# Optimization experiments

Hardware: AMD Instinct MI355X
Metric: run time of the kernel (lower is better)

Reference implementation:

```python
import jax, jax.numpy as jnp
import numpy as np

B, T, D, U = 32, 2048, 512, 512


def setup_inputs() -> dict:
    key = jax.random.key(0)
    ks = jax.random.split(key, 6)
    scale = 0.05
    return {
        "values": jax.random.normal(ks[0], (B, T, D), dtype=jnp.float32),
        "query": jax.random.normal(ks[1], (B, D), dtype=jnp.float32),
        "W1_w": jax.random.normal(ks[2], (D, U), dtype=jnp.float32) * scale,
        "W1_b": jnp.zeros((U,), dtype=jnp.float32),
        "W2_w": jax.random.normal(ks[3], (D, U), dtype=jnp.float32) * scale,
        "W2_b": jnp.zeros((U,), dtype=jnp.float32),
        "V_w": jax.random.normal(ks[4], (U, 1), dtype=jnp.float32) * scale,
        "V_b": jnp.zeros((1,), dtype=jnp.float32),
    }


def reference(values, query, W1_w, W1_b, W2_w, W2_b, V_w, V_b):
    # values: [B, T, D]; query: [B, D]
    proj_v = jnp.einsum("btd,du->btu", values, W1_w) + W1_b          # [B, T, U]
    proj_q = (query @ W2_w + W2_b)[:, None, :]                        # [B, 1, U]
    score = jnp.tanh(proj_v + proj_q) @ V_w + V_b                     # [B, T, 1]
    attention_weights = jax.nn.softmax(score, axis=1)                 # [B, T, 1]
    context_vector = jnp.sum(attention_weights * values, axis=1)      # [B, D]
    return context_vector, attention_weights
```

## Files before the change

kernel.cpp:

```cpp
#include <hip/hip_runtime.h>
#include <hip/hip_bf16.h>
#include <stdint.h>


#define B_DIM 32
#define T_DIM 2048
#define D_DIM 512
#define U_DIM 512
#define M_DIM (B_DIM * T_DIM)

typedef short bf16x8 __attribute__((ext_vector_type(8)));
typedef float f32x4 __attribute__((ext_vector_type(4)));

__device__ __forceinline__ float fast_tanh(float x) {
    float e = __expf(2.0f * x);
    return 1.0f - __fdividef(2.0f, e + 1.0f);
}

__device__ __forceinline__ short bf16r(float x) {
    unsigned u = __float_as_uint(x);
    u += 0x7fffu + ((u >> 16) & 1u);
    return (short)(u >> 16);
}

__device__ __forceinline__ bf16x8 pack8(float4 a, float4 b) {
    union { __hip_bfloat162 h[4]; bf16x8 v; } u;
    u.h[0] = __float22bfloat162_rn(make_float2(a.x, a.y));
    u.h[1] = __float22bfloat162_rn(make_float2(a.z, a.w));
    u.h[2] = __float22bfloat162_rn(make_float2(b.x, b.y));
    u.h[3] = __float22bfloat162_rn(make_float2(b.z, b.w));
    return u.v;
}

__device__ __forceinline__ void g2lds16(const void* g, void* lds) {
    auto gp = reinterpret_cast<const __attribute__((address_space(1))) unsigned int*>(
        reinterpret_cast<uintptr_t>(g));
    auto lp = reinterpret_cast<__attribute__((address_space(3))) unsigned int*>(
        (unsigned int)(uintptr_t)lds);
    __builtin_amdgcn_global_load_lds(gp, lp, 16, 0, 0);
}


__global__ void prep_kernel(const float* __restrict__ W1_w,
                            const float* __restrict__ W1_b,
                            const float* __restrict__ W2_w,
                            const float* __restrict__ W2_b,
                            const float* __restrict__ query,
                            unsigned short* __restrict__ W1T,
                            float* __restrict__ qb) {
    __shared__ float red[256];
    const int tid = threadIdx.x;
    if (blockIdx.x < 128) {
        int n = blockIdx.x * 256 + tid;
        int uu    = n & 255;
        int kc    = (n >> 8) & 3;
        int kstep = (n >> 10) & 15;
        int ut    = n >> 14;
        int u  = ut * 256 + uu;
        int k0 = kstep * 32 + kc * 8;
        bf16x8 pk;
#pragma unroll
        for (int j = 0; j < 8; ++j)
            pk[j] = bf16r(W1_w[(size_t)(k0 + j) * U_DIM + u]);
        ((bf16x8*)W1T)[n] = pk;
    } else {
        int bid = blockIdx.x - 128;
        int b  = bid >> 3;
        int ug = bid & 7;
        int u  = ug * 64 + (tid & 63);
        int dq = tid >> 6;
        const float* q  = query + b * D_DIM + dq * 128;
        const float* w2 = W2_w + (size_t)(dq * 128) * U_DIM + u;
        float acc = 0.f;
#pragma unroll 8
        for (int d = 0; d < 128; ++d)
            acc += q[d] * w2[(size_t)d * U_DIM];
        red[tid] = acc;
        __syncthreads();
        if (tid < 64) {
            qb[b * U_DIM + u] = red[tid] + red[tid + 64] + red[tid + 128]
                              + red[tid + 192] + W2_b[u] + W1_b[u];
        }
    }
}

__global__ __launch_bounds__(256, 2) void score_kernel(
        const float* __restrict__ values,
        const unsigned short* __restrict__ W1T,
        const float* __restrict__ qb,
        const float* __restrict__ Vw,
        float* __restrict__ sP) {
    __shared__ __align__(16) unsigned char smem[16384];

    const int tid  = threadIdx.x;
    const int lane = tid & 63;
    const int w    = tid >> 6;
    const int l15  = lane & 15;
    const int quad = lane >> 4;
    const int wr   = w >> 1, wc = w & 1;
    const int ut    = blockIdx.x & 1;
    const int mtile = blockIdx.x >> 1;
    const int mb    = mtile * 64;
    const int b     = mb >> 11;

    const float* arow0 = values + (size_t)(mb + wr * 32 + l15) * D_DIM + quad * 8;
    const float* arow1 = arow0 + 16 * D_DIM;

    f32x4 acc[2][8] = {};

    for (int ks = 0; ks < 16; ++ks) {
        float4 a00 = *(const float4*)(arow0 + ks * 32);
        float4 a01 = *(const float4*)(arow0 + ks * 32 + 4);
        float4 a10 = *(const float4*)(arow1 + ks * 32);
        float4 a11 = *(const float4*)(arow1 + ks * 32 + 4);

        __syncthreads();
        const unsigned short* src = W1T + (size_t)(ut * 16 + ks) * 8192;
#pragma unroll
        for (int i = 0; i < 4; ++i) {
            int unit = i * 256 + w * 64 + lane;
            g2lds16(src + (size_t)unit * 8, smem + unit * 16);
        }
        __syncthreads();

        bf16x8 a0 = pack8(a00, a01);
        bf16x8 a1 = pack8(a10, a11);
        const unsigned char* bbase = smem + (size_t)(quad * 256 + wc * 128 + l15) * 16;
#pragma unroll
        for (int ui = 0; ui < 8; ++ui) {
            bf16x8 bf = *(const bf16x8*)(bbase + ui * 256);
            acc[0][ui] = __builtin_amdgcn_mfma_f32_16x16x32_bf16(a0, bf, acc[0][ui], 0, 0, 0);
            acc[1][ui] = __builtin_amdgcn_mfma_f32_16x16x32_bf16(a1, bf, acc[1][ui], 0, 0, 0);
        }
    }

    const int ub = ut * 256 + wc * 128 + l15;
    float sm[2][4] = {};
#pragma unroll
    for (int ui = 0; ui < 8; ++ui) {
        const int u = ub + ui * 16;
        const float qv = qb[b * U_DIM + u];
        const float vw = Vw[u];
#pragma unroll
        for (int mt = 0; mt < 2; ++mt)
#pragma unroll
            for (int r = 0; r < 4; ++r)
                sm[mt][r] += fast_tanh(acc[mt][ui][r] + qv) * vw;
    }
#pragma unroll
    for (int mt = 0; mt < 2; ++mt)
#pragma unroll
        for (int r = 0; r < 4; ++r) {
            float v = sm[mt][r];
            v += __shfl_xor(v, 1, 64);
            v += __shfl_xor(v, 2, 64);
            v += __shfl_xor(v, 4, 64);
            v += __shfl_xor(v, 8, 64);
            sm[mt][r] = v;
        }
    if (l15 == 0) {
        const int slice = ut * 2 + wc;
#pragma unroll
        for (int mt = 0; mt < 2; ++mt)
#pragma unroll
            for (int r = 0; r < 4; ++r)
                sP[slice * M_DIM + mb + wr * 32 + mt * 16 + quad * 4 + r] = sm[mt][r];
    }
}

__global__ void softmax_kernel(const float* __restrict__ sP,
                               float* __restrict__ out) {
    const int b = blockIdx.x;
    const int tid = threadIdx.x;

    float v[8];
    float mx = -1e30f;
#pragma unroll
    for (int i = 0; i < 8; ++i) {
        int m = b * T_DIM + i * 256 + tid;
        v[i] = sP[m] + sP[M_DIM + m] + sP[2 * M_DIM + m] + sP[3 * M_DIM + m];
        mx = fmaxf(mx, v[i]);
    }
#pragma unroll
    for (int off = 1; off < 64; off <<= 1)
        mx = fmaxf(mx, __shfl_xor(mx, off, 64));
    __shared__ float redm[4];
    if ((tid & 63) == 0) redm[tid >> 6] = mx;
    __syncthreads();
    mx = fmaxf(fmaxf(redm[0], redm[1]), fmaxf(redm[2], redm[3]));

    float sum = 0.f;
#pragma unroll
    for (int i = 0; i < 8; ++i) {
        v[i] = __expf(v[i] - mx);
        sum += v[i];
    }
#pragma unroll
    for (int off = 1; off < 64; off <<= 1)
        sum += __shfl_xor(sum, off, 64);
    __shared__ float reds[4];
    if ((tid & 63) == 0) reds[tid >> 6] = sum;
    __syncthreads();
    sum = reds[0] + reds[1] + reds[2] + reds[3];

    const float inv = 1.0f / sum;
#pragma unroll
    for (int i = 0; i < 8; ++i)
        out[B_DIM * D_DIM + b * T_DIM + i * 256 + tid] = v[i] * inv;
}

__global__ void context_kernel(const float* __restrict__ values,
                               const float* __restrict__ weights,
                               float* __restrict__ P) {
    __shared__ float sw[64];
    __shared__ float red[512];
    const int tc = blockIdx.x;
    const int b  = blockIdx.y;
    const int tid = threadIdx.x;
    const int d4 = tid & 127;
    const int th = tid >> 7;

    if (tid < 64) sw[tid] = weights[b * T_DIM + tc * 64 + tid];
    __syncthreads();

    const float4* vb = (const float4*)(values + ((size_t)b * T_DIM + tc * 64) * D_DIM) + d4;
    float4 acc = {0.f, 0.f, 0.f, 0.f};
#pragma unroll 8
    for (int i = th; i < 64; i += 2) {
        float wv = sw[i];
        float4 vv = vb[(size_t)i * 128];
        acc.x += wv * vv.x; acc.y += wv * vv.y;
        acc.z += wv * vv.z; acc.w += wv * vv.w;
    }
    if (th == 1) ((float4*)red)[d4] = acc;
    __syncthreads();
    if (th == 0) {
        float4 o = ((float4*)red)[d4];
        acc.x += o.x; acc.y += o.y; acc.z += o.z; acc.w += o.w;
        *(float4*)(P + ((size_t)(b * 32 + tc)) * 512 + d4 * 4) = acc;
    }
}

__global__ void reduce_kernel(const float* __restrict__ P,
                              float* __restrict__ ctx) {
    const int g = blockIdx.x * 256 + threadIdx.x;
    const int b = g >> 9, d = g & 511;
    float s = 0.f;
#pragma unroll
    for (int tc = 0; tc < 32; ++tc)
        s += P[((size_t)(b * 32 + tc)) * 512 + d];
    ctx[g] = s;
}

extern "C" void kernel_launch(void* const* d_in, const int* in_sizes, int n_in,
                              void* d_out, int out_size, void* d_ws, size_t ws_size,
                              hipStream_t stream) {
    const float* values = (const float*)d_in[0];
    const float* query  = (const float*)d_in[1];
    const float* W1_w   = (const float*)d_in[2];
    const float* W1_b   = (const float*)d_in[3];
    const float* W2_w   = (const float*)d_in[4];
    const float* W2_b   = (const float*)d_in[5];
    const float* V_w    = (const float*)d_in[6];

    float* out = (float*)d_out;

    unsigned char* ws = (unsigned char*)d_ws;
    unsigned short* W1T = (unsigned short*)(ws);
    float* qb = (float*)(ws + 524288);
    float* sP = (float*)(ws + 524288 + 65536);
    float* P  = (float*)(ws + 524288 + 65536 + 1048576);

    prep_kernel<<<384, 256, 0, stream>>>(W1_w, W1_b, W2_w, W2_b, query, W1T, qb);
    score_kernel<<<2048, 256, 0, stream>>>(values, W1T, qb, V_w, sP);
    softmax_kernel<<<B_DIM, 256, 0, stream>>>(sP, out);
    context_kernel<<<dim3(32, B_DIM), 256, 0, stream>>>(values, out + B_DIM * D_DIM, P);
    reduce_kernel<<<64, 256, 0, stream>>>(P, out);
}
```

Before: 292.8 us.

## Pre-convert values to tiled bf16 and double-buffer score GEMM loads in LDS

The prep kernel now converts the whole values tensor to bf16 in an MFMA-friendly tiled layout. The score kernel then loads both A and B tiles into double-buffered LDS with async global-to-LDS copies, prefetching the next k-step while computing the current one. Each block now covers all 512 U columns with 512 threads, instead of two blocks splitting U, so values are read once per M tile. The cost is an extra full pass over values (read 128MB fp32, write 64MB bf16) and a larger LDS footprint.

New measurement: 330.0 us. 12.7% more time.

```diff
diff --git a/kernel.cpp b/kernel.cpp
--- a/kernel.cpp
+++ b/kernel.cpp
@@ -21,15 +21,6 @@
     unsigned u = __float_as_uint(x);
     u += 0x7fffu + ((u >> 16) & 1u);
     return (short)(u >> 16);
-}
-
-__device__ __forceinline__ bf16x8 pack8(float4 a, float4 b) {
-    union { __hip_bfloat162 h[4]; bf16x8 v; } u;
-    u.h[0] = __float22bfloat162_rn(make_float2(a.x, a.y));
-    u.h[1] = __float22bfloat162_rn(make_float2(a.z, a.w));
-    u.h[2] = __float22bfloat162_rn(make_float2(b.x, b.y));
-    u.h[3] = __float22bfloat162_rn(make_float2(b.z, b.w));
-    return u.v;
 }
 
 __device__ __forceinline__ void g2lds16(const void* g, void* lds) {
@@ -41,22 +32,36 @@
 }
 
 
-__global__ void prep_kernel(const float* __restrict__ W1_w,
+__global__ void prep_kernel(const float* __restrict__ values,
+                            const float* __restrict__ W1_w,
                             const float* __restrict__ W1_b,
                             const float* __restrict__ W2_w,
                             const float* __restrict__ W2_b,
                             const float* __restrict__ query,
+                            unsigned short* __restrict__ VA,
                             unsigned short* __restrict__ W1T,
                             float* __restrict__ qb) {
     __shared__ float red[256];
     const int tid = threadIdx.x;
-    if (blockIdx.x < 128) {
+    if (blockIdx.x < 16384) {
         int n = blockIdx.x * 256 + tid;
-        int uu    = n & 255;
-        int kc    = (n >> 8) & 3;
-        int kstep = (n >> 10) & 15;
-        int ut    = n >> 14;
-        int u  = ut * 256 + uu;
+        int mrow   = n & 63;
+        int kc     = (n >> 6) & 3;
+        int kstep  = (n >> 8) & 15;
+        int mblock = n >> 12;
+        const float* src = values + (size_t)(mblock * 64 + mrow) * D_DIM
+                                  + kstep * 32 + kc * 8;
+        float4 f0 = *(const float4*)(src);
+        float4 f1 = *(const float4*)(src + 4);
+        bf16x8 pk;
+        pk[0] = bf16r(f0.x); pk[1] = bf16r(f0.y); pk[2] = bf16r(f0.z); pk[3] = bf16r(f0.w);
+        pk[4] = bf16r(f1.x); pk[5] = bf16r(f1.y); pk[6] = bf16r(f1.z); pk[7] = bf16r(f1.w);
+        ((bf16x8*)VA)[n] = pk;
+    } else if (blockIdx.x < 16512) {
+        int n = (blockIdx.x - 16384) * 256 + tid;
+        int u     = n & 511;
+        int kc    = (n >> 9) & 3;
+        int kstep = n >> 11;
         int k0 = kstep * 32 + kc * 8;
         bf16x8 pk;
 #pragma unroll
@@ -64,7 +69,7 @@
             pk[j] = bf16r(W1_w[(size_t)(k0 + j) * U_DIM + u]);
         ((bf16x8*)W1T)[n] = pk;
     } else {
-        int bid = blockIdx.x - 128;
+        int bid = blockIdx.x - 16512;
         int b  = bid >> 3;
         int ug = bid & 7;
         int u  = ug * 64 + (tid & 63);
@@ -84,57 +89,68 @@
     }
 }
 
-__global__ __launch_bounds__(256, 2) void score_kernel(
-        const float* __restrict__ values,
+__global__ __launch_bounds__(512, 4) void score_kernel(
+        const unsigned short* __restrict__ VA,
         const unsigned short* __restrict__ W1T,
         const float* __restrict__ qb,
         const float* __restrict__ Vw,
         float* __restrict__ sP) {
-    __shared__ __align__(16) unsigned char smem[16384];
+    __shared__ __align__(16) unsigned char smemB[2][32768];
+    __shared__ __align__(16) unsigned char smemA[2][4096];
 
     const int tid  = threadIdx.x;
     const int lane = tid & 63;
     const int w    = tid >> 6;
     const int l15  = lane & 15;
     const int quad = lane >> 4;
-    const int wr   = w >> 1, wc = w & 1;
-    const int ut    = blockIdx.x & 1;
-    const int mtile = blockIdx.x >> 1;
-    const int mb    = mtile * 64;
-    const int b     = mb >> 11;
-
-    const float* arow0 = values + (size_t)(mb + wr * 32 + l15) * D_DIM + quad * 8;
-    const float* arow1 = arow0 + 16 * D_DIM;
+    const int wr   = w >> 2;
+    const int wc   = w & 3;
+    const int mb   = blockIdx.x * 64;
+    const int b    = mb >> 11;
+
+    const unsigned short* srcA = VA + (size_t)blockIdx.x * 16 * 2048;
+    const unsigned short* srcB = W1T;
+
+    if (tid < 256)
+        g2lds16(srcA + (size_t)tid * 8, smemA[0] + tid * 16);
+#pragma unroll
+    for (int i = 0; i < 4; ++i) {
+        int unit = i * 512 + tid;
+        g2lds16(srcB + (size_t)unit * 8, smemB[0] + unit * 16);
+    }
 
     f32x4 acc[2][8] = {};
 
     for (int ks = 0; ks < 16; ++ks) {
-        float4 a00 = *(const float4*)(arow0 + ks * 32);
-        float4 a01 = *(const float4*)(arow0 + ks * 32 + 4);
-        float4 a10 = *(const float4*)(arow1 + ks * 32);
-        float4 a11 = *(const float4*)(arow1 + ks * 32 + 4);
-
         __syncthreads();
-        const unsigned short* src = W1T + (size_t)(ut * 16 + ks) * 8192;
-#pragma unroll
-        for (int i = 0; i < 4; ++i) {
-            int unit = i * 256 + w * 64 + lane;
-            g2lds16(src + (size_t)unit * 8, smem + unit * 16);
-        }
-        __syncthreads();
-
-        bf16x8 a0 = pack8(a00, a01);
-        bf16x8 a1 = pack8(a10, a11);
-        const unsigned char* bbase = smem + (size_t)(quad * 256 + wc * 128 + l15) * 16;
+
+        if (ks < 15) {
+            const unsigned short* nA = srcA + (size_t)(ks + 1) * 2048;
+            const unsigned short* nB = srcB + (size_t)(ks + 1) * 16384;
+            unsigned char* bufA = smemA[(ks + 1) & 1];
+            unsigned char* bufB = smemB[(ks + 1) & 1];
+            if (tid < 256)
+                g2lds16(nA + (size_t)tid * 8, bufA + tid * 16);
+#pragma unroll
+            for (int i = 0; i < 4; ++i) {
+                int unit = i * 512 + tid;
+                g2lds16(nB + (size_t)unit * 8, bufB + unit * 16);
+            }
+        }
+
+        const unsigned char* aB = smemA[ks & 1] + quad * 1024 + (wr * 32 + l15) * 16;
+        bf16x8 a0 = *(const bf16x8*)(aB);
+        bf16x8 a1 = *(const bf16x8*)(aB + 256);
+        const unsigned char* bB = smemB[ks & 1] + (size_t)(quad * 512 + wc * 128 + l15) * 16;
 #pragma unroll
         for (int ui = 0; ui < 8; ++ui) {
-            bf16x8 bf = *(const bf16x8*)(bbase + ui * 256);
+            bf16x8 bf = *(const bf16x8*)(bB + ui * 256);
             acc[0][ui] = __builtin_amdgcn_mfma_f32_16x16x32_bf16(a0, bf, acc[0][ui], 0, 0, 0);
             acc[1][ui] = __builtin_amdgcn_mfma_f32_16x16x32_bf16(a1, bf, acc[1][ui], 0, 0, 0);
         }
     }
 
-    const int ub = ut * 256 + wc * 128 + l15;
+    const int ub = wc * 128 + l15;
     float sm[2][4] = {};
 #pragma unroll
     for (int ui = 0; ui < 8; ++ui) {
@@ -159,12 +175,11 @@
             sm[mt][r] = v;
         }
     if (l15 == 0) {
-        const int slice = ut * 2 + wc;
 #pragma unroll
         for (int mt = 0; mt < 2; ++mt)
 #pragma unroll
             for (int r = 0; r < 4; ++r)
-                sP[slice * M_DIM + mb + wr * 32 + mt * 16 + quad * 4 + r] = sm[mt][r];
+                sP[wc * M_DIM + mb + wr * 32 + mt * 16 + quad * 4 + r] = sm[mt][r];
     }
 }
 
@@ -266,13 +281,15 @@
     float* out = (float*)d_out;
 
     unsigned char* ws = (unsigned char*)d_ws;
-    unsigned short* W1T = (unsigned short*)(ws);
-    float* qb = (float*)(ws + 524288);
-    float* sP = (float*)(ws + 524288 + 65536);
-    float* P  = (float*)(ws + 524288 + 65536 + 1048576);
-
-    prep_kernel<<<384, 256, 0, stream>>>(W1_w, W1_b, W2_w, W2_b, query, W1T, qb);
-    score_kernel<<<2048, 256, 0, stream>>>(values, W1T, qb, V_w, sP);
+    unsigned short* VA  = (unsigned short*)(ws);
+    unsigned short* W1T = (unsigned short*)(ws + 67108864);
+    float* qb = (float*)(ws + 67108864 + 524288);
+    float* sP = (float*)(ws + 67108864 + 524288 + 65536);
+    float* P  = (float*)(ws + 67108864 + 524288 + 65536 + 1048576);
+
+    prep_kernel<<<16768, 256, 0, stream>>>(values, W1_w, W1_b, W2_w, W2_b,
+                                           query, VA, W1T, qb);
+    score_kernel<<<1024, 512, 0, stream>>>(VA, W1T, qb, V_w, sP);
     softmax_kernel<<<B_DIM, 256, 0, stream>>>(sP, out);
     context_kernel<<<dim3(32, B_DIM), 256, 0, stream>>>(values, out + B_DIM * D_DIM, P);
     reduce_kernel<<<64, 256, 0, stream>>>(P, out);
```
